# Performance work log

Measured on AMD Instinct MI355X. Metric: run time of the kernel, lower is better.

The kernel has to match this reference:

```python
import jax, jax.numpy as jnp
import numpy as np
from jax import lax

# static config matching init_kwargs
H, W = 128, 128
THETA_RES, RHO_RES = 1.0, 1.0
C_IN, C_OUT = 64, 64
A = int(np.round(180.0 / THETA_RES))            # num angle bins = 180
R = int(np.ceil(np.sqrt(H * H + W * W) / RHO_RES))  # num rho bins = 182


def _make_rho_idx():
    # rho bin index for every (angle, pixel); pixels flattened h-major (h*W + w)
    th = np.arange(A, dtype=np.float64) * THETA_RES * np.pi / 180.0
    hh, ww = np.meshgrid(np.arange(H), np.arange(W), indexing='ij')
    xs = (ww - W / 2.0).ravel()
    ys = (hh - H / 2.0).ravel()
    r = np.round((xs[None, :] * np.cos(th)[:, None]
                  + ys[None, :] * np.sin(th)[:, None]) / RHO_RES).astype(np.int32)
    r = r + R // 2
    return np.clip(r, 0, R - 1)  # [A, H*W] int32


def dht(x, rho_idx):
    # Hough scatter: [N,C,H,W] -> [N,C,A,R]
    N, C, h, w = x.shape
    xf = x.reshape(N * C, h * w).T  # [HW, NC]

    def step(_, idx_a):
        acc = jax.ops.segment_sum(xf, idx_a, num_segments=R)  # [R, NC]
        return None, acc

    _, ht = lax.scan(step, None, rho_idx)       # [A, R, NC]
    return ht.transpose(2, 0, 1).reshape(N, C, A, R)


def idht(ht, rho_idx):
    # inverse Hough gather (transpose of dht): [N,C,A,R] -> [N,C,H,W]
    N, C, a, r = ht.shape
    hf = ht.reshape(N * C, a, r).transpose(1, 0, 2)  # [A, NC, R]

    def step(acc, args):
        ht_a, idx_a = args
        return acc + ht_a[:, idx_a], None  # gather along rho -> [NC, HW]

    acc0 = jnp.zeros((N * C, H * W), ht.dtype)
    acc, _ = lax.scan(step, acc0, (hf, rho_idx))
    return acc.reshape(N, C, H, W)


def conv91_relu(x, w, b, groups):
    # Conv2d kernel (9,1), padding (4,0), stride 1 + ReLU
    y = lax.conv_general_dilated(x, w, (1, 1), [(4, 4), (0, 0)],
                                 dimension_numbers=('NCHW', 'OIHW', 'NCHW'),
                                 feature_group_count=groups)
    return jax.nn.relu(y + b[None, :, None, None])


def setup_inputs():
    key = jax.random.key(0)
    ks = jax.random.split(key, 7)
    N = 4
    x = jax.random.normal(ks[0], (N, C_IN, H, W), dtype=jnp.float32)
    s1 = 1.0 / np.sqrt(9.0)
    s2 = 1.0 / np.sqrt(9.0 * C_IN)
    w1 = jax.random.normal(ks[1], (C_IN, 1, 9, 1), jnp.float32) * s1
    b1 = jax.random.normal(ks[2], (C_IN,), jnp.float32) * 0.01
    w2 = jax.random.normal(ks[3], (C_IN, C_IN, 9, 1), jnp.float32) * s2
    b2 = jax.random.normal(ks[4], (C_IN,), jnp.float32) * 0.01
    w3 = jax.random.normal(ks[5], (C_OUT, C_IN, 9, 1), jnp.float32) * s2
    b3 = jax.random.normal(ks[6], (C_OUT,), jnp.float32) * 0.01
    rho_idx = jnp.asarray(_make_rho_idx())  # [A, H*W] int32, precomputed buffer
    return {"x": x, "rho_idx": rho_idx, "w1": w1, "b1": b1,
            "w2": w2, "b2": b2, "w3": w3, "b3": b3}


def reference(x, rho_idx, w1, b1, w2, b2, w3, b3):
    out = dht(x, rho_idx)                       # [N,C,A,R]
    out = conv91_relu(out, w1, b1, groups=C_IN) # grouped (9,1) conv
    out = conv91_relu(out, w2, b2, groups=1)
    out = conv91_relu(out, w3, b3, groups=1)
    return idht(out, rho_idx)                   # [N,C_OUT,H,W]
```

## Files before the change

kernel.cpp:

```cpp
#include <hip/hip_runtime.h>

typedef unsigned short ushort_t;
typedef __attribute__((ext_vector_type(8))) short short8;
typedef __attribute__((ext_vector_type(4))) float float4v;
typedef __attribute__((ext_vector_type(2))) float float2v;

#define HW 16384
#define A_BINS 180
#define R_BINS 182
#define AP 188
#define CCH 64
#define NB 4
#define NC 256
#define MROWS (A_BINS * R_BINS)
#define MPROWS (AP * R_BINS)
#define PADPX HW
#define PLSTRIDE 17664

static __device__ __forceinline__ float b2f(ushort_t u) {
    union { unsigned u32; float f; } c; c.u32 = ((unsigned)u) << 16; return c.f;
}
static __device__ __forceinline__ float u2f(unsigned u) {
    union { unsigned u32; float f; } c; c.u32 = u; return c.f;
}
static __device__ __forceinline__ ushort_t f2b(float f) {
    union { float f; unsigned u; } c; c.f = f;
    unsigned r = c.u + 0x7fffu + ((c.u >> 16) & 1u);
    return (ushort_t)(r >> 16);
}
static __device__ __forceinline__ void pkaccu(float2v& a, unsigned u) {
    float2v b; b.x = u2f(u << 16); b.y = u2f(u & 0xffff0000u);
    asm("v_pk_add_f32 %0, %1, %0" : "+v"(a) : "v"(b));
}

union PrepShared {
    float tile[64][65];
    struct {
        int hist[4][R_BINS];
        int tot[R_BINS];
        int offl[R_BINS + 1];
        int cur[4][R_BINS];
        ushort_t sp[PLSTRIDE];
    } c;
};

__global__ __launch_bounds__(256) void k_prep(const float* __restrict__ x,
                                              ushort_t* __restrict__ xT,
                                              ushort_t* __restrict__ ht0,
                                              ushort_t* __restrict__ bufA,
                                              ushort_t* __restrict__ bufB,
                                              const float* __restrict__ w2,
                                              const float* __restrict__ w3,
                                              ushort_t* __restrict__ w2b,
                                              ushort_t* __restrict__ w3b,
                                              const int* __restrict__ rho,
                                              int* __restrict__ offs,
                                              ushort_t* __restrict__ plist) {
    __shared__ PrepShared u;
    int blk = blockIdx.x, t = threadIdx.x;
    if (blk < 1024) {
        int lane = t & 63, g = t >> 6;
        int pBase = (blk & 255) * 64;
        int ncBase = (blk >> 8) * 64;
#pragma unroll
        for (int i = 0; i < 16; ++i) {
            int ncl = g + i * 4;
            u.tile[ncl][lane] = x[(size_t)(ncBase + ncl) * HW + pBase + lane];
        }
        __syncthreads();
#pragma unroll
        for (int i = 0; i < 16; ++i) {
            int pl = g + i * 4;
            xT[(size_t)(pBase + pl) * 256 + ncBase + lane] = f2b(u.tile[lane][pl]);
        }
        return;
    }
    if (blk < 1337) {
        int sblk = blk - 1024;
        if (sblk == 312) {
            if (t < 64) ((uint2*)(xT + (size_t)PADPX * NC))[t] = (uint2){0u, 0u};
            return;
        }
        if (sblk < 24) {
            int b = sblk >> 3, j = sblk & 7;
            int ap = (j < 4) ? j : (184 + (j - 4));
            ushort_t* base = (b == 0 ? ht0 : (b == 1 ? bufA : bufB));
            uint4* p = (uint4*)(base + (size_t)ap * (R_BINS * NC));
            int n16 = R_BINS * NC / 8;
            for (int i = t; i < n16; i += 256) p[i] = (uint4){0, 0, 0, 0};
            return;
        }
        int rep = sblk - 24;
        const float* w = (rep >= 144) ? w3 : w2;
        ushort_t* wb = (rep >= 144) ? w3b : w2b;
        int idx = (rep % 144) * 256 + t;
        int j = idx & 7;
        int lane = (idx >> 3) & 63;
        int cot = (idx >> 9) & 3;
        int h = (idx >> 11) & 1;
        int k = idx >> 12;
        int co = cot * 16 + (lane & 15);
        int ci = h * 32 + (lane >> 4) * 8 + j;
        wb[idx] = f2b(w[(co * 64 + ci) * 9 + k]);
        return;
    }
    int a = blk - 1337, lane = t & 63, wv = t >> 6;
    for (int i = t; i < 4 * R_BINS; i += 256) ((int*)u.c.hist)[i] = 0;
    __syncthreads();
    const int* rA = rho + (size_t)a * HW;
#pragma unroll 4
    for (int i = 0; i < 64; ++i) {
        int r = rA[t + i * 256];
        atomicAdd(&u.c.hist[wv][r], 1);
    }
    __syncthreads();
    if (t < R_BINS) u.c.tot[t] = u.c.hist[0][t] + u.c.hist[1][t] + u.c.hist[2][t] + u.c.hist[3][t];
    __syncthreads();
    if (wv == 0) {
        int b0 = lane * 3;
        int c0 = (b0     < R_BINS) ? ((u.c.tot[b0]     + 7) & ~7) : 0;
        int c1 = (b0 + 1 < R_BINS) ? ((u.c.tot[b0 + 1] + 7) & ~7) : 0;
        int c2 = (b0 + 2 < R_BINS) ? ((u.c.tot[b0 + 2] + 7) & ~7) : 0;
        int sum = c0 + c1 + c2, inc = sum;
#pragma unroll
        for (int d = 1; d < 64; d <<= 1) {
            int vv = __shfl_up(inc, d);
            if (lane >= d) inc += vv;
        }
        int excl = inc - sum;
        if (b0     < R_BINS) u.c.offl[b0]     = excl;
        if (b0 + 1 < R_BINS) u.c.offl[b0 + 1] = excl + c0;
        if (b0 + 2 < R_BINS) u.c.offl[b0 + 2] = excl + c0 + c1;
        if (lane == 63) u.c.offl[R_BINS] = inc;
    }
    __syncthreads();
    if (t < R_BINS) {
        int b = u.c.offl[t];
        u.c.cur[0][t] = b; b += u.c.hist[0][t];
        u.c.cur[1][t] = b; b += u.c.hist[1][t];
        u.c.cur[2][t] = b; b += u.c.hist[2][t];
        u.c.cur[3][t] = b;
    }
    if (t <= R_BINS) offs[a * (R_BINS + 1) + t] = u.c.offl[t];
    __syncthreads();
#pragma unroll 4
    for (int i = 0; i < 64; ++i) {
        int p = t + i * 256;
        int r = rA[p];
        int pos = atomicAdd(&u.c.cur[wv][r], 1);
        u.c.sp[pos] = (ushort_t)p;
    }
    __syncthreads();
    if (t < R_BINS) {
        int base = u.c.offl[t] + u.c.tot[t];
        int pend = u.c.offl[t + 1];
        for (int k = base; k < pend; ++k) u.c.sp[k] = (ushort_t)PADPX;
    }
    __syncthreads();
    int len = u.c.offl[R_BINS];
    const uint4* spv = (const uint4*)u.c.sp;
    uint4* plv = (uint4*)(plist + (size_t)a * PLSTRIDE);
    for (int i = t; i < len / 8; i += 256) plv[i] = spv[i];
}

__global__ __launch_bounds__(256, 4) void k_dht_g7(const ushort_t* __restrict__ xT,
                                                   const int* __restrict__ offs,
                                                   const ushort_t* __restrict__ plist,
                                                   ushort_t* __restrict__ ht0) {
    int ax = blockIdx.x;
    int a = ax >> 1, half = ax & 1;
    int part = blockIdx.y;
    int t = threadIdx.x, lane = t & 63, wv = t >> 6;
    int wslot = part * 4 + wv;
    int nl = lane & 15;
    unsigned lhb = (unsigned)nl * 16;
    unsigned shsel = (lane & 16) ? 16u : 0u;
    const char* xh = (const char*)xT + half * 256;
    const uint4* plq = (const uint4*)(plist + (size_t)a * PLSTRIDE);
    const int* offA = offs + a * (R_BINS + 1);
    size_t obase = (size_t)(a + 4) * (R_BINS * NC) + half * 128;
    for (int r = wslot; r < R_BINS; r += 64) {
        int off = __builtin_amdgcn_readfirstlane(offA[r]);
        int end = __builtin_amdgcn_readfirstlane(offA[r + 1]);
        float2v ac0 = (float2v){0.f, 0.f}, ac1 = (float2v){0.f, 0.f};
        float2v ac2 = (float2v){0.f, 0.f}, ac3 = (float2v){0.f, 0.f};
        int j = off;
        if (j < end) {
            uint4 w = plq[j >> 3];
            for (;;) {
                int jn = j + 8;
                uint4 wn = (uint4){0u, 0u, 0u, 0u};
                bool more = jn < end;
                if (more) wn = plq[jn >> 3];
                {
                    unsigned we = (lane & 32) ? w.y : w.x;
                    unsigned ps = (we >> shsel) & 0xffffu;
                    uint4 u = *(const uint4*)(xh + ((size_t)ps << 9) + lhb);
                    pkaccu(ac0, u.x); pkaccu(ac1, u.y);
                    pkaccu(ac2, u.z); pkaccu(ac3, u.w);
                }
                {
                    unsigned we = (lane & 32) ? w.w : w.z;
                    unsigned ps = (we >> shsel) & 0xffffu;
                    uint4 u = *(const uint4*)(xh + ((size_t)ps << 9) + lhb);
                    pkaccu(ac0, u.x); pkaccu(ac1, u.y);
                    pkaccu(ac2, u.z); pkaccu(ac3, u.w);
                }
                if (!more) break;
                w = wn; j = jn;
            }
        }
        float rs[8] = {ac0.x, ac0.y, ac1.x, ac1.y, ac2.x, ac2.y, ac3.x, ac3.y};
#pragma unroll
        for (int c = 0; c < 8; ++c) {
            rs[c] += __shfl_xor(rs[c], 16);
            rs[c] += __shfl_xor(rs[c], 32);
        }
        if (lane < 16) {
            uint4 o;
            o.x = (unsigned)f2b(rs[0]) | ((unsigned)f2b(rs[1]) << 16);
            o.y = (unsigned)f2b(rs[2]) | ((unsigned)f2b(rs[3]) << 16);
            o.z = (unsigned)f2b(rs[4]) | ((unsigned)f2b(rs[5]) << 16);
            o.w = (unsigned)f2b(rs[6]) | ((unsigned)f2b(rs[7]) << 16);
            *(uint4*)(ht0 + obase + (size_t)r * NC + nl * 8) = o;
        }
    }
}

__global__ __launch_bounds__(256) void k_conv1(const ushort_t* __restrict__ ht0,
                                               const float* __restrict__ w1,
                                               const float* __restrict__ b1,
                                               ushort_t* __restrict__ bufA) {
    int t = threadIdx.x, c = t & 63;
    int r = blockIdx.x;
    int a0 = blockIdx.y * 30;
    float wr[9];
#pragma unroll
    for (int k = 0; k < 9; ++k) wr[k] = w1[c * 9 + k];
    float bb = b1[c];
    const ushort_t* ip = ht0 + ((size_t)a0 * R_BINS + r) * NC + t;
    float v[38];
#pragma unroll
    for (int j = 0; j < 38; ++j) v[j] = b2f(ip[(size_t)j * (R_BINS * NC)]);
    ushort_t* op = bufA + ((size_t)(a0 + 4) * R_BINS + r) * NC + t;
#pragma unroll
    for (int i = 0; i < 30; ++i) {
        float s = bb;
#pragma unroll
        for (int k = 0; k < 9; ++k) s = fmaf(v[i + k], wr[k], s);
        op[(size_t)i * (R_BINS * NC)] = f2b(fmaxf(s, 0.f));
    }
}

__global__ __launch_bounds__(256) void k_gemm(const ushort_t* __restrict__ in,
                                              const ushort_t* __restrict__ wb,
                                              const float* __restrict__ bias,
                                              ushort_t* __restrict__ out,
                                              int outRowOff) {
    __shared__ ushort_t Bs[36864];
    int t = threadIdx.x, lane = t & 63, wv = t >> 6;
    {
        const uint4* src = (const uint4*)wb;
        uint4* dst = (uint4*)Bs;
        for (int i = t; i < 36864 / 8; i += 256) dst[i] = src[i];
    }
    __syncthreads();
    int m = lane & 15, q = lane >> 4;
    int n = blockIdx.y;
    int rowBase = blockIdx.x * 256 + wv * 64;
    const ushort_t* inN = in + n * 64;
    size_t rof[4];
#pragma unroll
    for (int tl = 0; tl < 4; ++tl) {
        int row = rowBase + tl * 16 + m;
        int rowc = row < MROWS ? row : (MROWS - 1);
        rof[tl] = (size_t)rowc * NC;
    }
    float4v acc[4][4];
#pragma unroll
    for (int tl = 0; tl < 4; ++tl)
#pragma unroll
        for (int i = 0; i < 4; ++i) acc[tl][i] = (float4v){0.f, 0.f, 0.f, 0.f};

#pragma unroll
    for (int k = 0; k < 9; ++k) {
#pragma unroll
        for (int h = 0; h < 2; ++h) {
            const ushort_t* base = inN + (size_t)k * (R_BINS * NC) + h * 32 + q * 8;
            short8 af0 = *(const short8*)(base + rof[0]);
            short8 af1 = *(const short8*)(base + rof[1]);
            short8 af2 = *(const short8*)(base + rof[2]);
            short8 af3 = *(const short8*)(base + rof[3]);
            const ushort_t* bl = Bs + (size_t)((k * 2 + h) * 4) * 512 + lane * 8;
            short8 b0 = *(const short8*)(bl);
            short8 b1v = *(const short8*)(bl + 512);
            short8 b2v = *(const short8*)(bl + 1024);
            short8 b3v = *(const short8*)(bl + 1536);
            acc[0][0] = __builtin_amdgcn_mfma_f32_16x16x32_bf16(af0, b0, acc[0][0], 0, 0, 0);
            acc[0][1] = __builtin_amdgcn_mfma_f32_16x16x32_bf16(af0, b1v, acc[0][1], 0, 0, 0);
            acc[0][2] = __builtin_amdgcn_mfma_f32_16x16x32_bf16(af0, b2v, acc[0][2], 0, 0, 0);
            acc[0][3] = __builtin_amdgcn_mfma_f32_16x16x32_bf16(af0, b3v, acc[0][3], 0, 0, 0);
            acc[1][0] = __builtin_amdgcn_mfma_f32_16x16x32_bf16(af1, b0, acc[1][0], 0, 0, 0);
            acc[1][1] = __builtin_amdgcn_mfma_f32_16x16x32_bf16(af1, b1v, acc[1][1], 0, 0, 0);
            acc[1][2] = __builtin_amdgcn_mfma_f32_16x16x32_bf16(af1, b2v, acc[1][2], 0, 0, 0);
            acc[1][3] = __builtin_amdgcn_mfma_f32_16x16x32_bf16(af1, b3v, acc[1][3], 0, 0, 0);
            acc[2][0] = __builtin_amdgcn_mfma_f32_16x16x32_bf16(af2, b0, acc[2][0], 0, 0, 0);
            acc[2][1] = __builtin_amdgcn_mfma_f32_16x16x32_bf16(af2, b1v, acc[2][1], 0, 0, 0);
            acc[2][2] = __builtin_amdgcn_mfma_f32_16x16x32_bf16(af2, b2v, acc[2][2], 0, 0, 0);
            acc[2][3] = __builtin_amdgcn_mfma_f32_16x16x32_bf16(af2, b3v, acc[2][3], 0, 0, 0);
            acc[3][0] = __builtin_amdgcn_mfma_f32_16x16x32_bf16(af3, b0, acc[3][0], 0, 0, 0);
            acc[3][1] = __builtin_amdgcn_mfma_f32_16x16x32_bf16(af3, b1v, acc[3][1], 0, 0, 0);
            acc[3][2] = __builtin_amdgcn_mfma_f32_16x16x32_bf16(af3, b2v, acc[3][2], 0, 0, 0);
            acc[3][3] = __builtin_amdgcn_mfma_f32_16x16x32_bf16(af3, b3v, acc[3][3], 0, 0, 0);
        }
    }

    ushort_t* outN = out + n * 64;
#pragma unroll
    for (int tl = 0; tl < 4; ++tl) {
#pragma unroll
        for (int cot = 0; cot < 4; ++cot) {
            int co = cot * 16 + m;
            float bv = bias[co];
#pragma unroll
            for (int i = 0; i < 4; ++i) {
                int rowD = rowBase + tl * 16 + q * 4 + i;
                float v = fmaxf(acc[tl][cot][i] + bv, 0.f);
                if (rowD < MROWS) outN[(size_t)(rowD + outRowOff) * NC + co] = f2b(v);
            }
        }
    }
}

union SharedIdht {
    struct {
        int rhoL[A_BINS * 32];
        ushort_t st[2][34 * 256];
    } s;
    float tile[256 * 33];
};

__global__ __launch_bounds__(512, 2) void k_idht(const ushort_t* __restrict__ buf3,
                                                 const int* __restrict__ rho,
                                                 float* __restrict__ outp) {
    __shared__ SharedIdht u;
    int t = threadIdx.x;
    int P0 = blockIdx.x * 32;
    int px = t >> 4;
    int ncg = t & 15;
    for (int i = t; i < A_BINS * 32; i += 512) {
        int a = i >> 5, p = i & 31;
        u.s.rhoL[i] = rho[(size_t)a * HW + P0 + p];
    }
    __syncthreads();
    float2v acc[8];
#pragma unroll
    for (int i = 0; i < 8; ++i) acc[i] = (float2v){0.f, 0.f};
    {
        int r0 = u.s.rhoL[0], r1 = u.s.rhoL[31];
        int rmin0 = r0 < r1 ? r0 : r1;
        int cnt0 = (r0 < r1 ? r1 - r0 : r0 - r1) + 1;
        const uint4* src = (const uint4*)(buf3 + (size_t)rmin0 * NC);
        uint4* dst = (uint4*)u.s.st[0];
        for (int i = t; i < cnt0 * 32; i += 512) dst[i] = src[i];
    }
    __syncthreads();

    for (int a = 0; a < A_BINS; ++a) {
        int cur = a & 1;
        uint4 pv0, pv1, pv2;
        bool g0 = false, g1 = false, g2 = false;
        if (a + 1 < A_BINS) {
            int r0 = u.s.rhoL[(a + 1) * 32], r1 = u.s.rhoL[(a + 1) * 32 + 31];
            int rminN = r0 < r1 ? r0 : r1;
            int lim = ((r0 < r1 ? r1 - r0 : r0 - r1) + 1) * 32;
            const uint4* src = (const uint4*)(buf3 + (size_t)(a + 1) * (R_BINS * NC)
                                              + (size_t)rminN * NC);
            g0 = t < lim; g1 = t + 512 < lim; g2 = t + 1024 < lim;
            if (g0) pv0 = src[t];
            if (g1) pv1 = src[t + 512];
            if (g2) pv2 = src[t + 1024];
        }
        {
            int r0 = u.s.rhoL[a * 32], r1 = u.s.rhoL[a * 32 + 31];
            int rmin = r0 < r1 ? r0 : r1;
            int row = u.s.rhoL[a * 32 + px] - rmin;
            const uint4* sp = (const uint4*)(u.s.st[cur] + row * 256 + ncg * 16);
            uint4 v0 = sp[0];
            uint4 v1 = sp[1];
            pkaccu(acc[0], v0.x); pkaccu(acc[1], v0.y);
            pkaccu(acc[2], v0.z); pkaccu(acc[3], v0.w);
            pkaccu(acc[4], v1.x); pkaccu(acc[5], v1.y);
            pkaccu(acc[6], v1.z); pkaccu(acc[7], v1.w);
        }
        if (a + 1 < A_BINS) {
            uint4* dst = (uint4*)u.s.st[cur ^ 1];
            if (g0) dst[t] = pv0;
            if (g1) dst[t + 512] = pv1;
            if (g2) dst[t + 1024] = pv2;
        }
        __syncthreads();
    }

#pragma unroll
    for (int k = 0; k < 8; ++k) {
        int nc = ncg * 16 + 2 * k;
        u.tile[nc * 33 + px] = acc[k].x;
        u.tile[(nc + 1) * 33 + px] = acc[k].y;
    }
    __syncthreads();
    int px2 = t & 31, nc0 = t >> 5;
    float* on = outp + P0 + px2;
#pragma unroll
    for (int k = 0; k < 16; ++k) {
        int nc = nc0 + k * 16;
        on[(size_t)nc * HW] = u.tile[nc * 33 + px2];
    }
}

extern "C" void kernel_launch(void* const* d_in, const int* in_sizes, int n_in,
                              void* d_out, int out_size, void* d_ws, size_t ws_size,
                              hipStream_t stream) {
    const float* x   = (const float*)d_in[0];
    const int*   rho = (const int*)d_in[1];
    const float* w1  = (const float*)d_in[2];
    const float* b1  = (const float*)d_in[3];
    const float* w2  = (const float*)d_in[4];
    const float* b2  = (const float*)d_in[5];
    const float* w3  = (const float*)d_in[6];
    const float* b3  = (const float*)d_in[7];
    float* outp = (float*)d_out;

    char* ws = (char*)d_ws;
    size_t off = 0;
    auto alloc = [&](size_t bytes) -> void* {
        void* p = ws + off;
        off = (off + bytes + 255) & ~(size_t)255;
        return p;
    };
    ushort_t* xT    = (ushort_t*)alloc((size_t)(HW + 8) * NC * 2);
    ushort_t* ht0   = (ushort_t*)alloc((size_t)AP * R_BINS * NC * 2);
    ushort_t* bufA  = (ushort_t*)alloc((size_t)AP * R_BINS * NC * 2);
    ushort_t* bufB  = (ushort_t*)alloc((size_t)AP * R_BINS * NC * 2);
    ushort_t* buf3  = (ushort_t*)alloc((size_t)A_BINS * R_BINS * NC * 2);
    ushort_t* w2b   = (ushort_t*)alloc(36864 * 2);
    ushort_t* w3b   = (ushort_t*)alloc(36864 * 2);
    int*      offs  = (int*)alloc((size_t)A_BINS * (R_BINS + 1) * 4);
    ushort_t* plist = (ushort_t*)alloc((size_t)A_BINS * PLSTRIDE * 2);

    k_prep<<<1517, 256, 0, stream>>>(x, xT, ht0, bufA, bufB, w2, w3, w2b, w3b,
                                     rho, offs, plist);
    k_dht_g7<<<dim3(360, 16), 256, 0, stream>>>(xT, offs, plist, ht0);
    k_conv1<<<dim3(R_BINS, 6), 256, 0, stream>>>(ht0, w1, b1, bufA);
    k_gemm<<<dim3(128, NB), 256, 0, stream>>>(bufA, w2b, b2, bufB, 728);
    k_gemm<<<dim3(128, NB), 256, 0, stream>>>(bufB, w3b, b3, buf3, 0);
    k_idht<<<dim3(512), 512, 0, stream>>>(buf3, rho, outp);
}
```

Baseline: 374.7 us.

## Prefetch idht angle slices two ahead with triple LDS buffer and padded rows

Moves the inverse Hough gather from double-buffered LDS staging with one-ahead global prefetch to triple buffering, issuing global loads two angles ahead so their latency overlaps more compute. LDS rows are padded to 528 bytes to cut bank conflicts, and each thread now reads two 16-byte chunks 256 bytes apart, which changes the channel mapping in the final transpose. This costs more registers and LDS, which may hurt occupancy at launch bounds of 512 threads and 2 blocks.

```diff
diff --git a/kernel.cpp b/kernel.cpp
--- a/kernel.cpp
+++ b/kernel.cpp
@@ -16,6 +16,7 @@
 #define MPROWS (AP * R_BINS)
 #define PADPX HW
 #define PLSTRIDE 17664
+#define ST_ROWB 528
 
 static __device__ __forceinline__ float b2f(ushort_t u) {
     union { unsigned u32; float f; } c; c.u32 = ((unsigned)u) << 16; return c.f;
@@ -335,7 +336,7 @@
 union SharedIdht {
     struct {
         int rhoL[A_BINS * 32];
-        ushort_t st[2][34 * 256];
+        ushort_t st[3][34 * 264];
     } s;
     float tile[256 * 33];
 };
@@ -356,57 +357,82 @@
     float2v acc[8];
 #pragma unroll
     for (int i = 0; i < 8; ++i) acc[i] = (float2v){0.f, 0.f};
+
     {
-        int r0 = u.s.rhoL[0], r1 = u.s.rhoL[31];
-        int rmin0 = r0 < r1 ? r0 : r1;
-        int cnt0 = (r0 < r1 ? r1 - r0 : r0 - r1) + 1;
+        int r0 = u.s.rhoL[0], r31 = u.s.rhoL[31];
+        int rmin0 = r0 < r31 ? r0 : r31;
+        int cnt0 = (r0 < r31 ? r31 - r0 : r0 - r31) + 1;
         const uint4* src = (const uint4*)(buf3 + (size_t)rmin0 * NC);
-        uint4* dst = (uint4*)u.s.st[0];
-        for (int i = t; i < cnt0 * 32; i += 512) dst[i] = src[i];
-    }
-    __syncthreads();
-
+        for (int i = t; i < cnt0 * 32; i += 512) {
+            uint4 v = src[i];
+            *(uint4*)((char*)u.s.st[0] + (i >> 5) * ST_ROWB + ((i & 31) << 4)) = v;
+        }
+    }
+    uint4 R1a = (uint4){0,0,0,0}, R1b = (uint4){0,0,0,0}, R1c = (uint4){0,0,0,0};
+    int limR1 = 0;
+    {
+        int r0 = u.s.rhoL[32], r31 = u.s.rhoL[63];
+        int rmin = r0 < r31 ? r0 : r31;
+        limR1 = ((r0 < r31 ? r31 - r0 : r0 - r31) + 1) * 32;
+        const uint4* src = (const uint4*)(buf3 + (size_t)(R_BINS * NC) + (size_t)rmin * NC);
+        if (t < limR1)        R1a = src[t];
+        if (t + 512 < limR1)  R1b = src[t + 512];
+        if (t + 1024 < limR1) R1c = src[t + 1024];
+    }
+    __syncthreads();
+
+    int bc = 0;
     for (int a = 0; a < A_BINS; ++a) {
-        int cur = a & 1;
-        uint4 pv0, pv1, pv2;
-        bool g0 = false, g1 = false, g2 = false;
-        if (a + 1 < A_BINS) {
-            int r0 = u.s.rhoL[(a + 1) * 32], r1 = u.s.rhoL[(a + 1) * 32 + 31];
-            int rminN = r0 < r1 ? r0 : r1;
-            int lim = ((r0 < r1 ? r1 - r0 : r0 - r1) + 1) * 32;
-            const uint4* src = (const uint4*)(buf3 + (size_t)(a + 1) * (R_BINS * NC)
-                                              + (size_t)rminN * NC);
-            g0 = t < lim; g1 = t + 512 < lim; g2 = t + 1024 < lim;
-            if (g0) pv0 = src[t];
-            if (g1) pv1 = src[t + 512];
-            if (g2) pv2 = src[t + 1024];
+        uint4 R2a = (uint4){0,0,0,0}, R2b = (uint4){0,0,0,0}, R2c = (uint4){0,0,0,0};
+        int limR2 = 0;
+        if (a + 2 < A_BINS) {
+            int r0 = u.s.rhoL[(a + 2) * 32], r31 = u.s.rhoL[(a + 2) * 32 + 31];
+            int rmin = r0 < r31 ? r0 : r31;
+            limR2 = ((r0 < r31 ? r31 - r0 : r0 - r31) + 1) * 32;
+            const uint4* src = (const uint4*)(buf3 + (size_t)(a + 2) * (R_BINS * NC)
+                                              + (size_t)rmin * NC);
+            if (t < limR2)        R2a = src[t];
+            if (t + 512 < limR2)  R2b = src[t + 512];
+            if (t + 1024 < limR2) R2c = src[t + 1024];
         }
         {
-            int r0 = u.s.rhoL[a * 32], r1 = u.s.rhoL[a * 32 + 31];
-            int rmin = r0 < r1 ? r0 : r1;
+            int r0 = u.s.rhoL[a * 32], r31 = u.s.rhoL[a * 32 + 31];
+            int rmin = r0 < r31 ? r0 : r31;
             int row = u.s.rhoL[a * 32 + px] - rmin;
-            const uint4* sp = (const uint4*)(u.s.st[cur] + row * 256 + ncg * 16);
-            uint4 v0 = sp[0];
-            uint4 v1 = sp[1];
+            const char* rowp = (const char*)u.s.st[bc] + row * ST_ROWB + (ncg << 4);
+            uint4 v0 = *(const uint4*)rowp;
+            uint4 v1 = *(const uint4*)(rowp + 256);
             pkaccu(acc[0], v0.x); pkaccu(acc[1], v0.y);
             pkaccu(acc[2], v0.z); pkaccu(acc[3], v0.w);
             pkaccu(acc[4], v1.x); pkaccu(acc[5], v1.y);
             pkaccu(acc[6], v1.z); pkaccu(acc[7], v1.w);
         }
+        int bn = bc + 1; if (bn == 3) bn = 0;
         if (a + 1 < A_BINS) {
-            uint4* dst = (uint4*)u.s.st[cur ^ 1];
-            if (g0) dst[t] = pv0;
-            if (g1) dst[t + 512] = pv1;
-            if (g2) dst[t + 1024] = pv2;
-        }
+            char* dst = (char*)u.s.st[bn];
+            if (t < limR1)
+                *(uint4*)(dst + (t >> 5) * ST_ROWB + ((t & 31) << 4)) = R1a;
+            if (t + 512 < limR1)
+                *(uint4*)(dst + ((t + 512) >> 5) * ST_ROWB + (((t + 512) & 31) << 4)) = R1b;
+            if (t + 1024 < limR1)
+                *(uint4*)(dst + ((t + 1024) >> 5) * ST_ROWB + (((t + 1024) & 31) << 4)) = R1c;
+        }
+        R1a = R2a; R1b = R2b; R1c = R2c; limR1 = limR2;
+        bc = bn;
         __syncthreads();
     }
 
 #pragma unroll
-    for (int k = 0; k < 8; ++k) {
-        int nc = ncg * 16 + 2 * k;
+    for (int k = 0; k < 4; ++k) {
+        int nc = ncg * 8 + 2 * k;
         u.tile[nc * 33 + px] = acc[k].x;
         u.tile[(nc + 1) * 33 + px] = acc[k].y;
+    }
+#pragma unroll
+    for (int k = 0; k < 4; ++k) {
+        int nc = 128 + ncg * 8 + 2 * k;
+        u.tile[nc * 33 + px] = acc[4 + k].x;
+        u.tile[(nc + 1) * 33 + px] = acc[4 + k].y;
     }
     __syncthreads();
     int px2 = t & 31, nc0 = t >> 5;
```

Result: no change. 374.8 us (+0.0%).
